# Optimization experiments

Measured on AMD Instinct MI355X. Metric: run time of the kernel, lower is better.

Reference implementation:

```python
import jax, jax.numpy as jnp
import numpy as np
from jax import lax

N = 2048
B = 8
CH = 10
START = 1
STOP = 65


def setup_inputs() -> dict:
    key = jax.random.key(0)
    ks = jax.random.split(key, 13)

    def g(k, s):
        return jax.random.normal(k, s, jnp.float32) * 0.05

    return {
        "x": jax.random.normal(ks[0], (B, 1, N, N), jnp.float32),
        "wl": g(ks[1], (CH // 2, 1, 3, N)), "bl": g(ks[2], (CH // 2,)),
        "wr": g(ks[3], (CH // 2, 1, N, 3)), "br": g(ks[4], (CH // 2,)),
        "wA": g(ks[5], (CH, CH, 3)), "bA": g(ks[6], (CH,)),
        "wB": g(ks[7], (CH, CH, 3)), "bB": g(ks[8], (CH,)),  # shared by layers 2&3 (torch list aliasing)
        "wT": g(ks[9], (CH, CH, 3)), "bT": g(ks[10], (CH,)),
        "wm": g(ks[11], (2, CH, 1)), "bm": g(ks[12], (2,)),
        "start": START, "stop": STOP,
    }


def _conv1d(h, w, b, pad):
    y = lax.conv_general_dilated(h, w, (1,), [(pad, pad)], dimension_numbers=("NCH", "OIH", "NCH"))
    return y + b[None, :, None]


def _forward(x, wl, bl, wr, br, wA, bA, wB, bB, wT, bT, wm, bm, start, stop):
    n = x.shape[-1]
    # scan_left: Conv2d kernel (3, n), padding (1, 0) -> (B, 5, n, 1) -> squeeze
    left_ = lax.conv_general_dilated(x, wl, (1, 1), [(1, 1), (0, 0)], dimension_numbers=("NCHW", "OIHW", "NCHW"))
    left_ = left_[..., 0] + bl[None, :, None]
    # scan_right: Conv2d kernel (n, 3), padding (0, 1) -> (B, 5, 1, n) -> squeeze
    right_ = lax.conv_general_dilated(x, wr, (1, 1), [(0, 0), (1, 1)], dimension_numbers=("NCHW", "OIHW", "NCHW"))
    right_ = right_[:, :, 0, :] + br[None, :, None]
    lr = jnp.concatenate([left_, right_], axis=1)  # (B, 10, n)
    h = jax.nn.relu(_conv1d(lr, wA, bA, 1))
    h = jax.nn.relu(_conv1d(h, wB, bB, 1))  # same weights twice: torch [conv, relu]*2 aliasing
    h = jax.nn.relu(_conv1d(h, wB, bB, 1))
    # ConvTranspose1d(k=3, stride=1, pad=1) == Conv1d with transposed, spatially-flipped kernel, pad=1
    wTc = jnp.flip(jnp.swapaxes(wT, 0, 1), -1)
    for _ in range(3):
        h = jax.nn.relu(_conv1d(h, wTc, bT, 1))
    m = jax.nn.sigmoid(_conv1d(h, wm, bm, 0))  # (B, 2, n)
    left, right = m[:, 0, :], m[:, 1, :]
    xs = x[:, 0]  # (B, n, n)
    preds = []
    for d in range(start, stop):  # static diagonal indices
        curr = jnp.exp(jnp.diagonal(xs, offset=d, axis1=1, axis2=2))  # (B, n-d)
        mass_in = curr[:, 1:] * right[:, 1:n - d] + curr[:, :-1] * left[:, d:n - 1]
        mass_out = right[:, 0:n - d - 1] + left[:, d + 1:n]
        p = jnp.log(mass_in / mass_out)
        preds.append(p - jnp.mean(p))  # scalar mean over batch+positions, as torch.mean
    return jnp.concatenate(preds, axis=1)  # ragged preds concatenated: (B, sum(n-d-1))


def reference(x, wl, bl, wr, br, wA, bA, wB, bB, wT, bT, wm, bm, start, stop):
    return _forward(x, wl, bl, wr, br, wA, bA, wB, bB, wT, bT, wm, bm, start, stop)
```

## Files before the change

kernel.cpp:

```cpp
#include <hip/hip_runtime.h>
#include <hip/hip_bf16.h>

#define NN 2048
#define BB 8
#define TROW 128928

__global__ __launch_bounds__(256) void k_left(const float* __restrict__ x,
                                              const float* __restrict__ wl,
                                              float* __restrict__ R,
                                              float* __restrict__ psum) {
    if (blockIdx.x == 0 && threadIdx.x < 64) psum[threadIdx.x] = 0.f;
    __shared__ float red[4][60 * 65];
    int b = blockIdx.x >> 7;
    int rbase = (blockIdx.x & 127) << 4;
    int wv = threadIdx.x >> 6, lane = threadIdx.x & 63;
    int r0 = rbase + wv * 4;
    const float* xp = x + ((size_t)(b * NN + r0)) * NN;

    float acc[4][15];
#pragma unroll
    for (int r = 0; r < 4; r++)
#pragma unroll
        for (int k = 0; k < 15; k++) acc[r][k] = 0.f;

    for (int seg = 0; seg < 8; seg++) {
        int j0 = seg * 256 + lane * 4;
        float4 xv[4];
#pragma unroll
        for (int r = 0; r < 4; r++) xv[r] = *(const float4*)(xp + (size_t)r * NN + j0);
#pragma unroll
        for (int k = 0; k < 15; k++) {
            float4 w4 = *(const float4*)(wl + (size_t)k * NN + j0);
#pragma unroll
            for (int r = 0; r < 4; r++) {
                acc[r][k] = fmaf(xv[r].x, w4.x, acc[r][k]);
                acc[r][k] = fmaf(xv[r].y, w4.y, acc[r][k]);
                acc[r][k] = fmaf(xv[r].z, w4.z, acc[r][k]);
                acc[r][k] = fmaf(xv[r].w, w4.w, acc[r][k]);
            }
        }
    }
#pragma unroll
    for (int r = 0; r < 4; r++)
#pragma unroll
        for (int k = 0; k < 15; k++) red[wv][(r * 15 + k) * 65 + lane] = acc[r][k];
    __syncthreads();
    if (lane < 60) {
        const float* rp = &red[wv][lane * 65];
        float s = 0.f;
#pragma unroll
        for (int j = 0; j < 64; j++) s += rp[j];
        int r = lane / 15, k = lane - r * 15;
        R[(size_t)(b * NN + r0 + r) * 16 + k] = s;
    }
}

__global__ __launch_bounds__(512) void k_right(const float* __restrict__ x,
                                               const float* __restrict__ wr,
                                               float* __restrict__ CSp) {
    __shared__ float wf[512 * 16];
    __shared__ float CS_l[15 * 256];
    int b = blockIdx.x >> 5;
    int rem = blockIdx.x & 31;
    int jc = rem >> 2, rc = rem & 3;
    int j0 = jc * 256, r0 = rc * 512;
    int tid = threadIdx.x;
    int wv = tid >> 6, lane = tid & 63;

    for (int idx = tid; idx < 512 * 15; idx += 512) {
        int hh = idx / 15, k = idx - hh * 15;
        int c = k / 3, dw = k - c * 3;
        wf[hh * 16 + k] = wr[c * (NN * 3) + (r0 + hh) * 3 + dw];
    }
    for (int idx = tid; idx < 15 * 256; idx += 512) CS_l[idx] = 0.f;
    __syncthreads();

    float acc[15][4];
#pragma unroll
    for (int k = 0; k < 15; k++)
#pragma unroll
        for (int e = 0; e < 4; e++) acc[k][e] = 0.f;

    const float* xp = x + ((size_t)b * NN + r0) * NN + j0 + lane * 4;
#pragma unroll 2
    for (int i = 0; i < 64; i++) {
        int rloc = wv + 8 * i;
        float4 xv = *(const float4*)(xp + (size_t)rloc * NN);
        const float* wrow = &wf[rloc * 16];
        float4 w0 = *(const float4*)(wrow);
        float4 w1 = *(const float4*)(wrow + 4);
        float4 w2 = *(const float4*)(wrow + 8);
        float4 w3 = *(const float4*)(wrow + 12);
        float wk[15] = {w0.x, w0.y, w0.z, w0.w, w1.x, w1.y, w1.z, w1.w,
                        w2.x, w2.y, w2.z, w2.w, w3.x, w3.y, w3.z};
#pragma unroll
        for (int k = 0; k < 15; k++) {
            acc[k][0] = fmaf(xv.x, wk[k], acc[k][0]);
            acc[k][1] = fmaf(xv.y, wk[k], acc[k][1]);
            acc[k][2] = fmaf(xv.z, wk[k], acc[k][2]);
            acc[k][3] = fmaf(xv.w, wk[k], acc[k][3]);
        }
    }
    int l4 = lane * 4;
#pragma unroll
    for (int k = 0; k < 15; k++)
#pragma unroll
        for (int e = 0; e < 4; e++) atomicAdd(&CS_l[k * 256 + l4 + e], acc[k][e]);
    __syncthreads();
    float* outp = CSp + (((size_t)rc * BB + b) * 16) * NN + j0;
    for (int idx = tid; idx < 15 * 256; idx += 512) {
        int k = idx >> 8, col = idx & 255;
        outp[(size_t)k * NN + col] = CS_l[idx];
    }
}

__global__ __launch_bounds__(256) void k_chainC(const float* __restrict__ R,
                                                const float* __restrict__ CSp,
                                                const float* __restrict__ bl,
                                                const float* __restrict__ br,
                                                const float* __restrict__ wA, const float* __restrict__ bA,
                                                const float* __restrict__ wB, const float* __restrict__ bB,
                                                const float* __restrict__ wT, const float* __restrict__ bT,
                                                const float* __restrict__ wm, const float* __restrict__ bm,
                                                float* __restrict__ LEFT, float* __restrict__ RIGHT) {
    __shared__ float buf0[10][144], buf1[10][144];
    __shared__ float W[3][10][10][3];
    __shared__ float Bs[3][10];
    __shared__ float Wm[2][10], Bm[2];
    int b = blockIdx.x >> 4;
    int c0 = (blockIdx.x & 15) << 7;
    int tid = threadIdx.x;

    for (int idx = tid; idx < 900; idx += 256) {
        int set = idx / 300, rem = idx - set * 300;
        int o = rem / 30, rem2 = rem - o * 30, c = rem2 / 3, kk = rem2 - c * 3;
        float u;
        if (set == 0) u = wA[o * 30 + c * 3 + kk];
        else if (set == 1) u = wB[o * 30 + c * 3 + kk];
        else u = wT[c * 30 + o * 3 + (2 - kk)];
        W[set][o][c][kk] = u;
    }
    if (tid < 30) {
        float v = (tid < 10) ? bA[tid] : (tid < 20) ? bB[tid - 10] : bT[tid - 20];
        Bs[tid / 10][tid % 10] = v;
    }
    if (tid < 20) Wm[tid / 10][tid % 10] = wm[tid];
    if (tid < 2) Bm[tid] = bm[tid];

    for (int idx = tid; idx < 1400; idx += 256) {
        int ch = idx / 140, p = idx - ch * 140;
        int g = c0 - 6 + p;
        float v = 0.f;
        if (g >= 0 && g < NN) {
            if (ch < 5) {
                v = bl[ch];
#pragma unroll
                for (int dh = 0; dh < 3; dh++) {
                    int r = g + dh - 1;
                    if (r >= 0 && r < NN) v += R[(size_t)(b * NN + r) * 16 + ch * 3 + dh];
                }
            } else {
                int c = ch - 5;
                v = br[c];
#pragma unroll
                for (int dw = 0; dw < 3; dw++) {
                    int j = g + dw - 1;
                    if (j >= 0 && j < NN) {
#pragma unroll
                        for (int rc = 0; rc < 4; rc++)
                            v += CSp[(((size_t)rc * BB + b) * 16 + c * 3 + dw) * NN + j];
                    }
                }
            }
        }
        buf0[ch][p] = v;
    }
    __syncthreads();

    float(*in)[144] = buf0;
    float(*out)[144] = buf1;
    for (int layer = 0; layer < 6; layer++) {
        int set = (layer == 0) ? 0 : (layer < 3 ? 1 : 2);
        int lo = layer + 1;
        for (int idx = tid; idx < 1400; idx += 256) {
            int o = idx / 140, p = idx - o * 140;
            if (p >= lo && p < 140 - lo) {
                float s = Bs[set][o];
#pragma unroll
                for (int c = 0; c < 10; c++) {
                    const float* ip = &in[c][p];
                    s = fmaf(ip[-1], W[set][o][c][0], s);
                    s = fmaf(ip[0], W[set][o][c][1], s);
                    s = fmaf(ip[1], W[set][o][c][2], s);
                }
                s = s > 0.f ? s : 0.f;
                int g = c0 - 6 + p;
                if (g < 0 || g >= NN) s = 0.f;
                out[o][p] = s;
            }
        }
        __syncthreads();
        float(*tmp)[144] = in; in = out; out = tmp;
    }
    {
        int idx = tid;
        int o = idx >> 7, pp = idx & 127;
        int p = 6 + pp;
        float s = Bm[o];
#pragma unroll
        for (int c = 0; c < 10; c++) s = fmaf(in[c][p], Wm[o][c], s);
        float sig = 1.f / (1.f + __expf(-s));
        (o ? RIGHT : LEFT)[b * NN + c0 + pp] = sig;
    }
}

__global__ __launch_bounds__(256) void k_diagmass(const float* __restrict__ x,
                                                  const float* __restrict__ LEFT,
                                                  const float* __restrict__ RIGHT,
                                                  float* __restrict__ P,
                                                  float* __restrict__ psum) {
    __shared__ float T[65][65];
    __shared__ float psl[64];
    int b = blockIdx.x >> 5;
    int i0 = (blockIdx.x & 31) << 6;
    int tid = threadIdx.x;

    for (int idx = tid; idx < 65 * 64; idx += 256) {
        int r = idx >> 6, dm1 = idx & 63;
        int row = i0 + r;
        int col = row + dm1 + 1;
        float v = 0.f;
        if (row < NN && col < NN) v = __expf(x[((size_t)b * NN + row) * NN + col]);
        T[r][dm1] = v;
    }
    __syncthreads();

    int wv = tid >> 6, lane = tid & 63;
    int i = i0 + lane;
    const float* lf = LEFT + b * NN;
    const float* rt = RIGHT + b * NN;
#pragma unroll
    for (int s = 0; s < 16; s++) {
        int dm1 = wv * 16 + s;
        int d = dm1 + 1;
        int L = (NN - 1) - d;
        float p = 0.f;
        if (i < L) {
            float mi = T[lane + 1][dm1] * rt[i + 1] + T[lane][dm1] * lf[d + i];
            float mo = rt[i] + lf[d + 1 + i];
            p = __logf(mi / mo);
            P[((size_t)dm1 * BB + b) * NN + i] = p;
        }
        float s64 = p;
        for (int off = 32; off; off >>= 1) s64 += __shfl_down(s64, off);
        if (lane == 0) psl[dm1] = s64;
    }
    __syncthreads();
    if (tid < 64) atomicAdd(&psum[tid], psl[tid]);
}

__global__ __launch_bounds__(1024) void k_out(const float* __restrict__ P,
                                              const float* __restrict__ psum,
                                              float* __restrict__ outp) {
    int dm1 = blockIdx.x >> 2, q = blockIdx.x & 3;
    int d = dm1 + 1;
    int L = (NN - 1) - d;
    int tid = threadIdx.x;
    int b2 = tid >> 9, ii = tid & 511;
    int i = q * 512 + ii;
    if (i >= L) return;
    float mean = psum[dm1] / (float)(8 * L);
    size_t off0 = (size_t)dm1 * (NN - 1) - (size_t)dm1 * (dm1 + 1) / 2;
#pragma unroll
    for (int bs = 0; bs < 4; bs++) {
        int b = b2 + bs * 2;
        outp[(size_t)b * TROW + off0 + i] = P[((size_t)dm1 * BB + b) * NN + i] - mean;
    }
}

extern "C" void kernel_launch(void* const* d_in, const int* in_sizes, int n_in,
                              void* d_out, int out_size, void* d_ws, size_t ws_size,
                              hipStream_t stream) {
    const float* x = (const float*)d_in[0];
    const float* wl = (const float*)d_in[1];
    const float* bl = (const float*)d_in[2];
    const float* wr = (const float*)d_in[3];
    const float* br = (const float*)d_in[4];
    const float* wA = (const float*)d_in[5];
    const float* bA = (const float*)d_in[6];
    const float* wB = (const float*)d_in[7];
    const float* bB = (const float*)d_in[8];
    const float* wT = (const float*)d_in[9];
    const float* bT = (const float*)d_in[10];
    const float* wm = (const float*)d_in[11];
    const float* bm = (const float*)d_in[12];

    float* ws = (float*)d_ws;
    float* R    = ws;
    float* CSp  = ws + 262144;
    float* LEFT = ws + 1310720;
    float* RIGHT= ws + 1327104;
    float* P    = ws + 1343488;
    float* psum = ws + 2392064;

    k_left<<<1024, 256, 0, stream>>>(x, wl, R, psum);
    k_right<<<256, 512, 0, stream>>>(x, wr, CSp);
    k_chainC<<<128, 256, 0, stream>>>(R, CSp, bl, br, wA, bA, wB, bB, wT, bT, wm, bm, LEFT, RIGHT);
    k_diagmass<<<256, 256, 0, stream>>>(x, LEFT, RIGHT, P, psum);
    k_out<<<256, 1024, 0, stream>>>(P, psum, (float*)d_out);
}
```

Baseline: 346.4 us.

## Restructure right-scan partitioning, precompute padded weights, add partial-sum reduction kernel

k_left now uses twice as many blocks with 2 rows per wave instead of 4, and also writes the right-scan weights into a padded 16-wide buffer. k_right drops the shared-memory weight staging and LDS atomics: each thread owns 2 columns over a 128-row chunk and writes 16 row-chunk partials directly. A new k_csum kernel sums those partials so k_chainC reads a single reduced array. The aim is better occupancy and no LDS atomic contention, in exchange for an extra launch and more partial-sum traffic.

```diff
diff --git a/kernel.cpp b/kernel.cpp
--- a/kernel.cpp
+++ b/kernel.cpp
@@ -7,32 +7,44 @@
 
 __global__ __launch_bounds__(256) void k_left(const float* __restrict__ x,
                                               const float* __restrict__ wl,
+                                              const float* __restrict__ wr,
                                               float* __restrict__ R,
+                                              float* __restrict__ WF,
                                               float* __restrict__ psum) {
     if (blockIdx.x == 0 && threadIdx.x < 64) psum[threadIdx.x] = 0.f;
-    __shared__ float red[4][60 * 65];
-    int b = blockIdx.x >> 7;
-    int rbase = (blockIdx.x & 127) << 4;
+    if (blockIdx.x < 128) {
+        int idx = blockIdx.x * 256 + threadIdx.x;
+        int h = idx >> 4, k = idx & 15;
+        float v = 0.f;
+        if (k < 15) {
+            int c = k / 3, dw = k - c * 3;
+            v = wr[c * (NN * 3) + h * 3 + dw];
+        }
+        WF[idx] = v;
+    }
+    __shared__ float red[4][30 * 65];
+    int b = blockIdx.x >> 8;
+    int rg = blockIdx.x & 255;
     int wv = threadIdx.x >> 6, lane = threadIdx.x & 63;
-    int r0 = rbase + wv * 4;
+    int r0 = rg * 8 + wv * 2;
     const float* xp = x + ((size_t)(b * NN + r0)) * NN;
 
-    float acc[4][15];
-#pragma unroll
-    for (int r = 0; r < 4; r++)
+    float acc[2][15];
+#pragma unroll
+    for (int r = 0; r < 2; r++)
 #pragma unroll
         for (int k = 0; k < 15; k++) acc[r][k] = 0.f;
 
     for (int seg = 0; seg < 8; seg++) {
         int j0 = seg * 256 + lane * 4;
-        float4 xv[4];
-#pragma unroll
-        for (int r = 0; r < 4; r++) xv[r] = *(const float4*)(xp + (size_t)r * NN + j0);
+        float4 xv[2];
+#pragma unroll
+        for (int r = 0; r < 2; r++) xv[r] = *(const float4*)(xp + (size_t)r * NN + j0);
 #pragma unroll
         for (int k = 0; k < 15; k++) {
             float4 w4 = *(const float4*)(wl + (size_t)k * NN + j0);
 #pragma unroll
-            for (int r = 0; r < 4; r++) {
+            for (int r = 0; r < 2; r++) {
                 acc[r][k] = fmaf(xv[r].x, w4.x, acc[r][k]);
                 acc[r][k] = fmaf(xv[r].y, w4.y, acc[r][k]);
                 acc[r][k] = fmaf(xv[r].z, w4.z, acc[r][k]);
@@ -41,11 +53,11 @@
         }
     }
 #pragma unroll
-    for (int r = 0; r < 4; r++)
+    for (int r = 0; r < 2; r++)
 #pragma unroll
         for (int k = 0; k < 15; k++) red[wv][(r * 15 + k) * 65 + lane] = acc[r][k];
     __syncthreads();
-    if (lane < 60) {
+    if (lane < 30) {
         const float* rp = &red[wv][lane * 65];
         float s = 0.f;
 #pragma unroll
@@ -56,66 +68,59 @@
 }
 
 __global__ __launch_bounds__(512) void k_right(const float* __restrict__ x,
-                                               const float* __restrict__ wr,
+                                               const float* __restrict__ WF,
                                                float* __restrict__ CSp) {
-    __shared__ float wf[512 * 16];
-    __shared__ float CS_l[15 * 256];
     int b = blockIdx.x >> 5;
     int rem = blockIdx.x & 31;
-    int jc = rem >> 2, rc = rem & 3;
-    int j0 = jc * 256, r0 = rc * 512;
-    int tid = threadIdx.x;
-    int wv = tid >> 6, lane = tid & 63;
-
-    for (int idx = tid; idx < 512 * 15; idx += 512) {
-        int hh = idx / 15, k = idx - hh * 15;
-        int c = k / 3, dw = k - c * 3;
-        wf[hh * 16 + k] = wr[c * (NN * 3) + (r0 + hh) * 3 + dw];
-    }
-    for (int idx = tid; idx < 15 * 256; idx += 512) CS_l[idx] = 0.f;
-    __syncthreads();
-
-    float acc[15][4];
-#pragma unroll
-    for (int k = 0; k < 15; k++)
-#pragma unroll
-        for (int e = 0; e < 4; e++) acc[k][e] = 0.f;
-
-    const float* xp = x + ((size_t)b * NN + r0) * NN + j0 + lane * 4;
-#pragma unroll 2
-    for (int i = 0; i < 64; i++) {
-        int rloc = wv + 8 * i;
-        float4 xv = *(const float4*)(xp + (size_t)rloc * NN);
-        const float* wrow = &wf[rloc * 16];
-        float4 w0 = *(const float4*)(wrow);
-        float4 w1 = *(const float4*)(wrow + 4);
-        float4 w2 = *(const float4*)(wrow + 8);
-        float4 w3 = *(const float4*)(wrow + 12);
-        float wk[15] = {w0.x, w0.y, w0.z, w0.w, w1.x, w1.y, w1.z, w1.w,
-                        w2.x, w2.y, w2.z, w2.w, w3.x, w3.y, w3.z};
-#pragma unroll
-        for (int k = 0; k < 15; k++) {
-            acc[k][0] = fmaf(xv.x, wk[k], acc[k][0]);
-            acc[k][1] = fmaf(xv.y, wk[k], acc[k][1]);
-            acc[k][2] = fmaf(xv.z, wk[k], acc[k][2]);
-            acc[k][3] = fmaf(xv.w, wk[k], acc[k][3]);
-        }
-    }
-    int l4 = lane * 4;
-#pragma unroll
-    for (int k = 0; k < 15; k++)
-#pragma unroll
-        for (int e = 0; e < 4; e++) atomicAdd(&CS_l[k * 256 + l4 + e], acc[k][e]);
-    __syncthreads();
-    float* outp = CSp + (((size_t)rc * BB + b) * 16) * NN + j0;
-    for (int idx = tid; idx < 15 * 256; idx += 512) {
-        int k = idx >> 8, col = idx & 255;
-        outp[(size_t)k * NN + col] = CS_l[idx];
-    }
+    int jc = rem >> 4, rc = rem & 15;
+    int r0 = rc * 128;
+    int w = threadIdx.x >> 6, lane = threadIdx.x & 63;
+    int c0 = jc * 1024 + w * 128 + lane * 2;
+    const float* xp = x + ((size_t)b * NN + r0) * NN + c0;
+
+    float acc[15][2];
+#pragma unroll
+    for (int k = 0; k < 15; k++) { acc[k][0] = 0.f; acc[k][1] = 0.f; }
+
+    for (int rb = 0; rb < 16; rb++) {
+        float2 xv[8];
+#pragma unroll
+        for (int q = 0; q < 8; q++)
+            xv[q] = *(const float2*)(xp + (size_t)(rb * 8 + q) * NN);
+#pragma unroll
+        for (int q = 0; q < 8; q++) {
+            const float* wrow = WF + (size_t)(r0 + rb * 8 + q) * 16;
+#pragma unroll
+            for (int k = 0; k < 15; k++) {
+                float wk = wrow[k];
+                acc[k][0] = fmaf(xv[q].x, wk, acc[k][0]);
+                acc[k][1] = fmaf(xv[q].y, wk, acc[k][1]);
+            }
+        }
+    }
+    float* outp = CSp + ((size_t)(rc * BB + b) * 16) * NN + c0;
+#pragma unroll
+    for (int k = 0; k < 15; k++) {
+        float2 v; v.x = acc[k][0]; v.y = acc[k][1];
+        *(float2*)(outp + (size_t)k * NN) = v;
+    }
+}
+
+__global__ __launch_bounds__(256) void k_csum(const float* __restrict__ CSp,
+                                              float* __restrict__ CS) {
+    int vid = blockIdx.x * 256 + threadIdx.x;
+    const float4* src = (const float4*)CSp;
+    float4 s = src[vid];
+#pragma unroll
+    for (int rc = 1; rc < 16; rc++) {
+        float4 v = src[vid + rc * 65536];
+        s.x += v.x; s.y += v.y; s.z += v.z; s.w += v.w;
+    }
+    ((float4*)CS)[vid] = s;
 }
 
 __global__ __launch_bounds__(256) void k_chainC(const float* __restrict__ R,
-                                                const float* __restrict__ CSp,
+                                                const float* __restrict__ CS,
                                                 const float* __restrict__ bl,
                                                 const float* __restrict__ br,
                                                 const float* __restrict__ wA, const float* __restrict__ bA,
@@ -165,11 +170,8 @@
 #pragma unroll
                 for (int dw = 0; dw < 3; dw++) {
                     int j = g + dw - 1;
-                    if (j >= 0 && j < NN) {
-#pragma unroll
-                        for (int rc = 0; rc < 4; rc++)
-                            v += CSp[(((size_t)rc * BB + b) * 16 + c * 3 + dw) * NN + j];
-                    }
+                    if (j >= 0 && j < NN)
+                        v += CS[((size_t)b * 16 + c * 3 + dw) * NN + j];
                 }
             }
         }
@@ -298,14 +300,17 @@
     float* ws = (float*)d_ws;
     float* R    = ws;
     float* CSp  = ws + 262144;
-    float* LEFT = ws + 1310720;
-    float* RIGHT= ws + 1327104;
-    float* P    = ws + 1343488;
-    float* psum = ws + 2392064;
-
-    k_left<<<1024, 256, 0, stream>>>(x, wl, R, psum);
-    k_right<<<256, 512, 0, stream>>>(x, wr, CSp);
-    k_chainC<<<128, 256, 0, stream>>>(R, CSp, bl, br, wA, bA, wB, bB, wT, bT, wm, bm, LEFT, RIGHT);
+    float* WF   = ws + 4456448;
+    float* CS   = ws + 4489216;
+    float* LEFT = ws + 4751360;
+    float* RIGHT= ws + 4767744;
+    float* P    = ws + 4784128;
+    float* psum = ws + 5832704;
+
+    k_left<<<2048, 256, 0, stream>>>(x, wl, wr, R, WF, psum);
+    k_right<<<256, 512, 0, stream>>>(x, WF, CSp);
+    k_csum<<<256, 256, 0, stream>>>(CSp, CS);
+    k_chainC<<<128, 256, 0, stream>>>(R, CS, bl, br, wA, bA, wB, bB, wT, bT, wm, bm, LEFT, RIGHT);
     k_diagmass<<<256, 256, 0, stream>>>(x, LEFT, RIGHT, P, psum);
     k_out<<<256, 1024, 0, stream>>>(P, psum, (float*)d_out);
 }
```

New measurement: 329.6 us. -4.8%, faster.
